# Kernel optimization log

Measured on AMD Instinct MI355X. Metric: run time of the kernel, lower is better.

The kernel has to match this reference:

```python
import jax, jax.numpy as jnp
import numpy as np

N_NODES = 100000
N_EDGES = 3200000
IN_CH = 128
HID = 128
N_CLASSES = 32
N_GRAPHS = 256


def gcn_conv(x, W, b, src, dst, n_nodes):
    """PyG GCNConv: add self-loops, symmetric deg^-1/2 normalization,
    linear transform, gather-scatter aggregation, bias."""
    xw = x @ W  # [N, out]
    loop = jnp.arange(n_nodes, dtype=src.dtype)
    s = jnp.concatenate([src, loop])  # sources incl. self-loops
    d = jnp.concatenate([dst, loop])  # targets incl. self-loops
    deg = jax.ops.segment_sum(jnp.ones_like(d, dtype=xw.dtype), d,
                              num_segments=n_nodes)
    dinv = jnp.where(deg > 0, jax.lax.rsqrt(deg), 0.0)
    norm = dinv[s] * dinv[d]  # [E+N]
    msgs = xw[s] * norm[:, None]  # gather + scale
    out = jax.ops.segment_sum(msgs, d, num_segments=n_nodes)  # scatter-add
    return out + b


def global_mean_pool(x, batch, n_graphs):
    sums = jax.ops.segment_sum(x, batch, num_segments=n_graphs)
    cnt = jax.ops.segment_sum(jnp.ones((x.shape[0],), x.dtype), batch,
                              num_segments=n_graphs)
    return sums / jnp.maximum(cnt, 1.0)[:, None]


def setup_inputs() -> dict:
    key = jax.random.key(0)
    ks = jax.random.split(key, 9)
    x = jax.random.normal(ks[0], (N_NODES, IN_CH), dtype=jnp.float32)
    edge_index = jax.random.randint(ks[1], (2, N_EDGES), 0, N_NODES, dtype=jnp.int32)
    batch = jnp.sort(jax.random.randint(ks[2], (N_NODES,), 0, N_GRAPHS, dtype=jnp.int32))
    s1 = 1.0 / np.sqrt(IN_CH)
    s2 = 1.0 / np.sqrt(HID)
    W1 = jax.random.uniform(ks[3], (IN_CH, HID), jnp.float32, -s1, s1)
    b1 = jnp.zeros((HID,), jnp.float32)
    W2 = jax.random.uniform(ks[4], (HID, HID), jnp.float32, -s2, s2)
    b2 = jnp.zeros((HID,), jnp.float32)
    Wfc = jax.random.uniform(ks[5], (HID, N_CLASSES), jnp.float32, -s2, s2)
    bfc = jax.random.uniform(ks[6], (N_CLASSES,), jnp.float32, -s2, s2)
    return {"x": x, "edge_index": edge_index, "batch": batch,
            "W1": W1, "b1": b1, "W2": W2, "b2": b2, "Wfc": Wfc, "bfc": bfc}


def reference(x, edge_index, batch, W1, b1, W2, b2, Wfc, bfc):
    src, dst = edge_index[0], edge_index[1]
    h = jax.nn.relu(gcn_conv(x, W1, b1, src, dst, N_NODES))
    h = jax.nn.relu(gcn_conv(h, W2, b2, src, dst, N_NODES))
    g = global_mean_pool(h, batch, N_GRAPHS)  # [G, HID]
    return g @ Wfc + bfc  # [G, N_CLASSES]
```

## Files before the change

### kernel.cpp

```cpp
#include <hip/hip_runtime.h>
#include <hip/hip_bf16.h>
#include <hip/hip_fp16.h>

static constexpr int CH     = 128;
static constexpr int NCLS   = 32;
static constexpr int NGRAPH = 256;

static constexpr int BSHIFT = 8;
static constexpr int BW     = 1 << BSHIFT;
static constexpr int MAXB   = 512;

typedef _Float16 half8 __attribute__((ext_vector_type(8)));
typedef _Float16 half4 __attribute__((ext_vector_type(4)));
typedef float    f32x4 __attribute__((ext_vector_type(4)));
typedef float    f32x2 __attribute__((ext_vector_type(2)));

static constexpr float FP8_SCALE = 64.0f;
static constexpr float FP8_INV   = 1.0f / 64.0f;

__device__ __forceinline__ f32x2 dec8(unsigned short u) {
  return __builtin_amdgcn_cvt_pk_f32_fp8((int)u, false);
}
__device__ __forceinline__ unsigned char enc8(float v) {
  return (unsigned char)(__builtin_amdgcn_cvt_pk_fp8_f32(v, v, 0, false) & 0xFF);
}

__global__ __launch_bounds__(256) void k_init_wt(
    int* __restrict__ gcur, int CAP, int NBUCK, int* __restrict__ xzero,
    const float* __restrict__ W1, const float* __restrict__ W2,
    _Float16* __restrict__ WhT1, _Float16* __restrict__ WhT2) {
  int t = threadIdx.x;
  if (blockIdx.x == 0) {
    for (int i = t; i < NBUCK; i += 256) gcur[i] = i * CAP;
    if (t < 32) xzero[t] = 0;
    return;
  }
  int i = (blockIdx.x - 1) * 256 + t;
  const float* W = (i < CH * CH) ? W1 : W2;
  _Float16* T   = (i < CH * CH) ? WhT1 : WhT2;
  int j = i & (CH * CH - 1);
  int k = j >> 7, n = j & 127;
  T[n * CH + k] = (_Float16)W[j];
}

__global__ __launch_bounds__(1024) void k_scatter(
    const int* __restrict__ src, const int* __restrict__ dst,
    int* __restrict__ gcur, int* __restrict__ ebuf, int E) {
  __shared__ int bcnt[MAXB];
  __shared__ int bbase[MAXB];
  int t = threadIdx.x;
  if (t < MAXB) bcnt[t] = 0;
  __syncthreads();
  int base = blockIdx.x * 8192;
  int s_[8], d_[8], r_[8];
  #pragma unroll
  for (int j = 0; j < 8; ++j) {
    int i = base + j * 1024 + t;
    if (i < E) {
      s_[j] = src[i];
      d_[j] = dst[i];
      r_[j] = atomicAdd(&bcnt[d_[j] >> BSHIFT], 1);
    }
  }
  __syncthreads();
  if (t < MAXB && bcnt[t]) bbase[t] = atomicAdd(&gcur[t], bcnt[t]);
  __syncthreads();
  #pragma unroll
  for (int j = 0; j < 8; ++j) {
    int i = base + j * 1024 + t;
    if (i < E) {
      int b = d_[j] >> BSHIFT;
      int p = ((d_[j] & (BW - 1)) << 17) | s_[j];
      ebuf[bbase[b] + r_[j]] = p;
    }
  }
}

__global__ __launch_bounds__(1024) void k_build(
    const int* __restrict__ ebuf, const int* __restrict__ gcur,
    int* __restrict__ offs, int* __restrict__ oend,
    float* __restrict__ dinv, int* __restrict__ csr, int N, int CAP) {
  __shared__ int sdeg[BW];
  __shared__ int sscan[BW];
  int b = blockIdx.x;
  int t = threadIdx.x;
  int lo = b << BSHIFT;
  int e0 = b * CAP;
  int e1 = gcur[b];

  if (t < BW) sdeg[t] = 0;
  __syncthreads();
  for (int e = e0 + t; e < e1; e += 1024)
    atomicAdd(&sdeg[ebuf[e] >> 17], 1);
  __syncthreads();
  if (t < BW) sscan[t] = (sdeg[t] + 3) & ~3;
  __syncthreads();
  for (int st = 1; st < BW; st <<= 1) {
    int v = (t < BW && t >= st) ? sscan[t - st] : 0;
    __syncthreads();
    if (t < BW) sscan[t] += v;
    __syncthreads();
  }
  if (t < BW) {
    int deg  = sdeg[t];
    int pdeg = (deg + 3) & ~3;
    int ex = b * CAP + sscan[t] - pdeg;
    int n = lo + t;
    if (n < N) {
      offs[n] = ex;
      oend[n] = ex + deg;
      dinv[n] = 1.0f / sqrtf((float)(deg + 1));
      for (int q = deg; q < pdeg; ++q) csr[ex + q] = N;
    }
    sscan[t] = ex;
  }
  __syncthreads();
  for (int e = e0 + t; e < e1; e += 1024) {
    int p = ebuf[e];
    int pos = atomicAdd(&sscan[p >> 17], 1);
    csr[pos] = p & 0x1FFFF;
  }
}

__device__ __forceinline__ void stage_w(const _Float16* __restrict__ WhT,
                                        _Float16 (*Ws)[136], int tid) {
  #pragma unroll
  for (int l = 0; l < 8; ++l) {
    int idx = tid + l * 256;
    int n = idx >> 4, k8 = (idx & 15) << 3;
    *(half8*)&Ws[n][k8] = *(const half8*)(WhT + n * CH + k8);
  }
}

__device__ __forceinline__ void gemm_core64(
    const _Float16 (*As)[136], const _Float16 (*Ws)[136],
    const float* __restrict__ dinv, unsigned char* __restrict__ C,
    int row0, int M, int tid) {
  int lane = tid & 63, wave = tid >> 6;
  int quad = lane >> 4, sub = lane & 15;
  int m0 = wave * 16;

  f32x4 acc[8];
  #pragma unroll
  for (int j = 0; j < 8; ++j) acc[j] = (f32x4){0.f, 0.f, 0.f, 0.f};

  #pragma unroll
  for (int kc = 0; kc < 4; ++kc) {
    int ko = kc * 32 + quad * 8;
    half8 a = *(const half8*)&As[m0 + sub][ko];
    #pragma unroll
    for (int nt = 0; nt < 8; ++nt) {
      half8 b = *(const half8*)&Ws[nt * 16 + sub][ko];
      acc[nt] = __builtin_amdgcn_mfma_f32_16x16x32_f16(a, b, acc[nt], 0, 0, 0);
    }
  }
  #pragma unroll
  for (int r = 0; r < 4; ++r) {
    int row = row0 + m0 + quad * 4 + r;
    if (row < M) {
      float d = dinv[row] * FP8_SCALE;
      #pragma unroll
      for (int nt = 0; nt < 8; ++nt)
        C[(size_t)row * CH + nt * 16 + sub] = enc8(acc[nt][r] * d);
    }
  }
}

__global__ __launch_bounds__(256) void k_gemm_f32(
    const float* __restrict__ A, const _Float16* __restrict__ WhT,
    const float* __restrict__ dinv, unsigned char* __restrict__ C, int M) {
  __shared__ _Float16 As[64][136];
  __shared__ _Float16 Ws[128][136];
  int tid = threadIdx.x;
  int row0 = blockIdx.x * 64;
  #pragma unroll
  for (int l = 0; l < 8; ++l) {
    int idx = tid + l * 256;
    int r = idx >> 5, c4 = (idx & 31) << 2;
    int rr = row0 + r; if (rr >= M) rr = M - 1;
    float4 v = *(const float4*)(A + (size_t)rr * CH + c4);
    half4 hv = { (_Float16)v.x, (_Float16)v.y, (_Float16)v.z, (_Float16)v.w };
    *(half4*)&As[r][c4] = hv;
  }
  stage_w(WhT, Ws, tid);
  __syncthreads();
  gemm_core64(As, Ws, dinv, C, row0, M, tid);
}

__global__ __launch_bounds__(256) void k_gemm_f16(
    const _Float16* __restrict__ A, const _Float16* __restrict__ WhT,
    const float* __restrict__ dinv, unsigned char* __restrict__ C, int M) {
  __shared__ _Float16 As[64][136];
  __shared__ _Float16 Ws[128][136];
  int tid = threadIdx.x;
  int row0 = blockIdx.x * 64;
  #pragma unroll
  for (int l = 0; l < 4; ++l) {
    int idx = tid + l * 256;
    int r = idx >> 4, c8 = (idx & 15) << 3;
    int rr = row0 + r; if (rr >= M) rr = M - 1;
    *(half8*)&As[r][c8] = *(const half8*)(A + (size_t)rr * CH + c8);
  }
  stage_w(WhT, Ws, tid);
  __syncthreads();
  gemm_core64(As, Ws, dinv, C, row0, M, tid);
}

__global__ __launch_bounds__(256) void k_agg(
    const unsigned char* __restrict__ xs, const int* __restrict__ csr,
    const int* __restrict__ offs, const int* __restrict__ oend,
    const float* __restrict__ dinv, const float* __restrict__ bias,
    __half* __restrict__ out, int N) {
  int wid0  = blockIdx.x * 4 + (threadIdx.x >> 6);
  int lane  = threadIdx.x & 63;
  int wstep = gridDim.x * 4;
  unsigned int lane2 = (unsigned int)lane << 1;
  float2 bxy = *(const float2*)(bias + 2 * lane);

  auto g = [&](int s) -> unsigned short {
    return *(const unsigned short*)(xs + (((unsigned int)s << 7) | lane2));
  };

  for (int wid = wid0; wid * 2 < N; wid += wstep) {
    int nA = wid * 2, nB = nA + 1;
    bool hasB = (nB < N);

    int eA = offs[nA];
    int cA = (oend[nA] - eA + 3) >> 2;
    int eB = hasB ? offs[nB] : eA;
    int cB = hasB ? ((oend[nB] - eB + 3) >> 2) : 0;

    f32x2 aA0 = dec8(g(nA));
    f32x2 aA1 = {0.f, 0.f};
    f32x2 aB0 = {0.f, 0.f}, aB1 = {0.f, 0.f};
    if (hasB) aB0 = dec8(g(nB));

    if (cA >= 2 && cB >= 2) {
      int4 ca0 = *(const int4*)(csr + eA);
      int4 ca1 = *(const int4*)(csr + eA + 4);
      int4 cb0 = *(const int4*)(csr + eB);
      int4 cb1 = *(const int4*)(csr + eB + 4);
      do {
        unsigned short uA0 = g(ca0.x), uA1 = g(ca0.y), uA2 = g(ca0.z), uA3 = g(ca0.w);
        unsigned short uA4 = g(ca1.x), uA5 = g(ca1.y), uA6 = g(ca1.z), uA7 = g(ca1.w);
        unsigned short uB0 = g(cb0.x), uB1 = g(cb0.y), uB2 = g(cb0.z), uB3 = g(cb0.w);
        unsigned short uB4 = g(cb1.x), uB5 = g(cb1.y), uB6 = g(cb1.z), uB7 = g(cb1.w);
        eA += 8; eB += 8; cA -= 2; cB -= 2;
        int4 na0 = *(const int4*)(csr + eA);
        int4 na1 = *(const int4*)(csr + eA + 4);
        int4 nb0 = *(const int4*)(csr + eB);
        int4 nb1 = *(const int4*)(csr + eB + 4);
        aA0 += dec8(uA0); aA1 += dec8(uA1); aA0 += dec8(uA2); aA1 += dec8(uA3);
        aA0 += dec8(uA4); aA1 += dec8(uA5); aA0 += dec8(uA6); aA1 += dec8(uA7);
        aB0 += dec8(uB0); aB1 += dec8(uB1); aB0 += dec8(uB2); aB1 += dec8(uB3);
        aB0 += dec8(uB4); aB1 += dec8(uB5); aB0 += dec8(uB6); aB1 += dec8(uB7);
        ca0 = na0; ca1 = na1; cb0 = nb0; cb1 = nb1;
      } while (cA >= 2 && cB >= 2);
    }

    auto drain = [&](int e, int c, f32x2& a0, f32x2& a1) {
      while (c >= 2) {
        int4 q0 = *(const int4*)(csr + e);
        int4 q1 = *(const int4*)(csr + e + 4);
        unsigned short u0 = g(q0.x), u1 = g(q0.y), u2 = g(q0.z), u3 = g(q0.w);
        unsigned short u4 = g(q1.x), u5 = g(q1.y), u6 = g(q1.z), u7 = g(q1.w);
        a0 += dec8(u0); a1 += dec8(u1); a0 += dec8(u2); a1 += dec8(u3);
        a0 += dec8(u4); a1 += dec8(u5); a0 += dec8(u6); a1 += dec8(u7);
        e += 8; c -= 2;
      }
      if (c > 0) {
        int4 q0 = *(const int4*)(csr + e);
        unsigned short u0 = g(q0.x), u1 = g(q0.y), u2 = g(q0.z), u3 = g(q0.w);
        a0 += dec8(u0); a1 += dec8(u1); a0 += dec8(u2); a1 += dec8(u3);
      }
    };
    drain(eA, cA, aA0, aA1);
    if (hasB) drain(eB, cB, aB0, aB1);

    {
      f32x2 s = aA0 + aA1;
      float dn = dinv[nA] * FP8_INV;
      float rx = fmaf(s[0], dn, bxy.x);
      float ry = fmaf(s[1], dn, bxy.y);
      ((__half2*)out)[(size_t)nA * 64 + lane] =
          __floats2half2_rn(fmaxf(rx, 0.f), fmaxf(ry, 0.f));
    }
    if (hasB) {
      f32x2 s = aB0 + aB1;
      float dn = dinv[nB] * FP8_INV;
      float rx = fmaf(s[0], dn, bxy.x);
      float ry = fmaf(s[1], dn, bxy.y);
      ((__half2*)out)[(size_t)nB * 64 + lane] =
          __floats2half2_rn(fmaxf(rx, 0.f), fmaxf(ry, 0.f));
    }
  }
}

__global__ __launch_bounds__(128) void k_pool(
    const __half* __restrict__ h, const int* __restrict__ batch,
    float* __restrict__ gsum, int* __restrict__ gstart,
    int* __restrict__ gend, int N) {
  int ch = threadIdx.x;
  int n0 = blockIdx.x * 128;
  int n1 = n0 + 128; if (n1 > N) n1 = N;
  if (n0 >= N) return;
  for (int n = n0 + ch; n < n1; n += 128) {
    int g = batch[n];
    if (n == 0 || batch[n - 1] != g) gstart[g] = n;
    if (n == N - 1 || batch[n + 1] != g) gend[g] = n + 1;
  }
  float acc = 0.f;
  int curg = batch[n0];
  for (int n = n0; n < n1; ++n) {
    int g = batch[n];
    if (g != curg) {
      atomicAdd(&gsum[curg * CH + ch], acc);
      acc = 0.f; curg = g;
    }
    acc += __half2float(h[(size_t)n * CH + ch]);
  }
  atomicAdd(&gsum[curg * CH + ch], acc);
}

__global__ __launch_bounds__(64) void k_fc(
    const float* __restrict__ gsum, const int* __restrict__ gstart,
    const int* __restrict__ gend, const float* __restrict__ Wfc,
    const float* __restrict__ bfc, float* __restrict__ outp) {
  int g = blockIdx.x;
  int j = threadIdx.x;
  if (j >= NCLS) return;
  int cnt = gend[g] - gstart[g];
  float invc = 1.0f / fmaxf((float)cnt, 1.0f);
  float acc = 0.0f;
  for (int c = 0; c < CH; ++c)
    acc = fmaf(gsum[g * CH + c], Wfc[c * NCLS + j], acc);
  outp[g * NCLS + j] = fmaf(acc, invc, bfc[j]);
}

extern "C" void kernel_launch(void* const* d_in, const int* in_sizes, int n_in,
                              void* d_out, int out_size, void* d_ws, size_t ws_size,
                              hipStream_t stream) {
  const float* x    = (const float*)d_in[0];
  const int*   ei   = (const int*)d_in[1];
  const int*   batch= (const int*)d_in[2];
  const float* W1   = (const float*)d_in[3];
  const float* b1   = (const float*)d_in[4];
  const float* W2   = (const float*)d_in[5];
  const float* b2   = (const float*)d_in[6];
  const float* Wfc  = (const float*)d_in[7];
  const float* bfc  = (const float*)d_in[8];
  float* outp = (float*)d_out;

  const int N = in_sizes[0] / CH;
  const int E = in_sizes[1] / 2;
  const int* src = ei;
  const int* dst = ei + E;
  const int NBUCK = (N + BW - 1) >> BSHIFT;
  int CAP = (E / NBUCK) + (E / NBUCK) / 8 + 1280;
  CAP = (CAP + 3) & ~3;

  char* w = (char*)d_ws;
  size_t o = 0;
  auto carve = [&](size_t bytes) -> void* {
    o = (o + 255) & ~(size_t)255;
    void* p = w + o;
    o += bytes;
    return p;
  };
  float*    gsum   = (float*)   carve((size_t)NGRAPH * CH * 4);
  int*      gstart = (int*)     carve((size_t)NGRAPH * 4);
  int*      gend   = (int*)     carve((size_t)NGRAPH * 4);
  size_t zbytes = o;
  int*      offs   = (int*)     carve((size_t)N * 4);
  int*      oendb  = (int*)     carve((size_t)N * 4);
  int*      gcur   = (int*)     carve(MAXB * 4);
  int*      csr    = (int*)     carve((size_t)NBUCK * CAP * 4);
  float*    dinv   = (float*)   carve((size_t)N * 4);
  _Float16* WhT1   = (_Float16*)carve((size_t)CH * CH * 2);
  _Float16* WhT2   = (_Float16*)carve((size_t)CH * CH * 2);
  unsigned char* xsbuf = (unsigned char*)carve((size_t)(N + 1) * CH);
  __half*   hbuf   = (__half*)  carve((size_t)N * CH * 2);
  (void)ws_size;

  int* ebuf = (int*)hbuf;

  (void)hipMemsetAsync(gsum, 0, zbytes, stream);

  const int GB64 = (N + 63) / 64;
  const int GB   = (N + 127) / 128;
  int AB = (N + 7) / 8;
  if (AB > 2048) AB = 2048;

  k_init_wt<<<129, 256, 0, stream>>>(gcur, CAP, NBUCK,
                                     (int*)(xsbuf + (size_t)N * CH),
                                     W1, W2, WhT1, WhT2);
  k_scatter<<<(E + 8191) / 8192, 1024, 0, stream>>>(src, dst, gcur, ebuf, E);
  k_build  <<<NBUCK, 1024, 0, stream>>>(ebuf, gcur, offs, oendb, dinv, csr, N, CAP);

  k_gemm_f32<<<GB64, 256, 0, stream>>>(x, WhT1, dinv, xsbuf, N);
  k_agg<<<AB, 256, 0, stream>>>(xsbuf, csr, offs, oendb, dinv, b1, hbuf, N);
  k_gemm_f16<<<GB64, 256, 0, stream>>>((const _Float16*)hbuf, WhT2, dinv, xsbuf, N);
  k_agg<<<AB, 256, 0, stream>>>(xsbuf, csr, offs, oendb, dinv, b2, hbuf, N);

  k_pool<<<GB, 128, 0, stream>>>(hbuf, batch, gsum, gstart, gend, N);
  k_fc<<<NGRAPH, 64, 0, stream>>>(gsum, gstart, gend, Wfc, bfc, outp);
  (void)out_size; (void)n_in;
}
```

Before: 350.0 us.

## Fuse setup kernels, split edges across half-waves in agg, fuse pool and fc

Removes k_init_wt by folding the weight transpose into k_build and the zeroing into k_scatter. A memset of gcur replaces precomputed bucket bases, and offsets are now relative. The aggregation kernel now has each half-wave process alternate edges with 4-byte gathers (4 fp8 channels per lane), combining the halves with a cross-half shuffle. Pooling and the final FC are fused into one per-graph kernel that uses a binary search on the sorted batch array instead of atomics. This cuts launches and atomics, but the agg path adds shuffles and predicated lanes, and the pool now has only 256 blocks.

```diff
diff --git a/kernel.cpp b/kernel.cpp
--- a/kernel.cpp
+++ b/kernel.cpp
@@ -18,37 +18,18 @@
 static constexpr float FP8_SCALE = 64.0f;
 static constexpr float FP8_INV   = 1.0f / 64.0f;
 
-__device__ __forceinline__ f32x2 dec8(unsigned short u) {
-  return __builtin_amdgcn_cvt_pk_f32_fp8((int)u, false);
-}
 __device__ __forceinline__ unsigned char enc8(float v) {
   return (unsigned char)(__builtin_amdgcn_cvt_pk_fp8_f32(v, v, 0, false) & 0xFF);
 }
 
-__global__ __launch_bounds__(256) void k_init_wt(
-    int* __restrict__ gcur, int CAP, int NBUCK, int* __restrict__ xzero,
-    const float* __restrict__ W1, const float* __restrict__ W2,
-    _Float16* __restrict__ WhT1, _Float16* __restrict__ WhT2) {
-  int t = threadIdx.x;
-  if (blockIdx.x == 0) {
-    for (int i = t; i < NBUCK; i += 256) gcur[i] = i * CAP;
-    if (t < 32) xzero[t] = 0;
-    return;
-  }
-  int i = (blockIdx.x - 1) * 256 + t;
-  const float* W = (i < CH * CH) ? W1 : W2;
-  _Float16* T   = (i < CH * CH) ? WhT1 : WhT2;
-  int j = i & (CH * CH - 1);
-  int k = j >> 7, n = j & 127;
-  T[n * CH + k] = (_Float16)W[j];
-}
-
 __global__ __launch_bounds__(1024) void k_scatter(
     const int* __restrict__ src, const int* __restrict__ dst,
-    int* __restrict__ gcur, int* __restrict__ ebuf, int E) {
+    int* __restrict__ gcur, int* __restrict__ ebuf, int E, int CAP,
+    int* __restrict__ xzero) {
   __shared__ int bcnt[MAXB];
   __shared__ int bbase[MAXB];
   int t = threadIdx.x;
+  if (blockIdx.x == 0 && t < 32) xzero[t] = 0;
   if (t < MAXB) bcnt[t] = 0;
   __syncthreads();
   int base = blockIdx.x * 8192;
@@ -71,7 +52,7 @@
     if (i < E) {
       int b = d_[j] >> BSHIFT;
       int p = ((d_[j] & (BW - 1)) << 17) | s_[j];
-      ebuf[bbase[b] + r_[j]] = p;
+      ebuf[b * CAP + bbase[b] + r_[j]] = p;
     }
   }
 }
@@ -79,14 +60,26 @@
 __global__ __launch_bounds__(1024) void k_build(
     const int* __restrict__ ebuf, const int* __restrict__ gcur,
     int* __restrict__ offs, int* __restrict__ oend,
-    float* __restrict__ dinv, int* __restrict__ csr, int N, int CAP) {
+    float* __restrict__ dinv, int* __restrict__ csr, int N, int CAP,
+    const float* __restrict__ W1, const float* __restrict__ W2,
+    _Float16* __restrict__ WhT1, _Float16* __restrict__ WhT2) {
   __shared__ int sdeg[BW];
   __shared__ int sscan[BW];
   int b = blockIdx.x;
   int t = threadIdx.x;
+
+  int gi = b * 1024 + t;
+  if (gi < 2 * CH * CH) {
+    const float* W = (gi < CH * CH) ? W1 : W2;
+    _Float16* T   = (gi < CH * CH) ? WhT1 : WhT2;
+    int j = gi & (CH * CH - 1);
+    int k = j >> 7, n = j & 127;
+    T[n * CH + k] = (_Float16)W[j];
+  }
+
   int lo = b << BSHIFT;
   int e0 = b * CAP;
-  int e1 = gcur[b];
+  int e1 = e0 + gcur[b];
 
   if (t < BW) sdeg[t] = 0;
   __syncthreads();
@@ -207,18 +200,19 @@
 }
 
 __global__ __launch_bounds__(256) void k_agg(
-    const unsigned char* __restrict__ xs, const int* __restrict__ csr,
+    const unsigned int* __restrict__ xs32, const int* __restrict__ csr,
     const int* __restrict__ offs, const int* __restrict__ oend,
     const float* __restrict__ dinv, const float* __restrict__ bias,
     __half* __restrict__ out, int N) {
+  int lane  = threadIdx.x & 63;
   int wid0  = blockIdx.x * 4 + (threadIdx.x >> 6);
-  int lane  = threadIdx.x & 63;
   int wstep = gridDim.x * 4;
-  unsigned int lane2 = (unsigned int)lane << 1;
-  float2 bxy = *(const float2*)(bias + 2 * lane);
-
-  auto g = [&](int s) -> unsigned short {
-    return *(const unsigned short*)(xs + (((unsigned int)s << 7) | lane2));
+  int e = lane >> 5;
+  unsigned int c = lane & 31;
+  float4 bb = *(const float4*)(bias + c * 4);
+
+  auto G = [&](int s) -> unsigned int {
+    return xs32[((unsigned int)s << 5) | c];
   };
 
   for (int wid = wid0; wid * 2 < N; wid += wstep) {
@@ -230,10 +224,22 @@
     int eB = hasB ? offs[nB] : eA;
     int cB = hasB ? ((oend[nB] - eB + 3) >> 2) : 0;
 
-    f32x2 aA0 = dec8(g(nA));
-    f32x2 aA1 = {0.f, 0.f};
-    f32x2 aB0 = {0.f, 0.f}, aB1 = {0.f, 0.f};
-    if (hasB) aB0 = dec8(g(nB));
+    f32x2 a0 = {0.f, 0.f}, a1 = {0.f, 0.f};
+    f32x2 b0 = {0.f, 0.f}, b1 = {0.f, 0.f};
+    if (e == 0) {
+      unsigned int ow = G(nA);
+      a0 = __builtin_amdgcn_cvt_pk_f32_fp8((int)ow, false);
+      a1 = __builtin_amdgcn_cvt_pk_f32_fp8((int)ow, true);
+      if (hasB) {
+        unsigned int ob = G(nB);
+        b0 = __builtin_amdgcn_cvt_pk_f32_fp8((int)ob, false);
+        b1 = __builtin_amdgcn_cvt_pk_f32_fp8((int)ob, true);
+      }
+    }
+
+    #define ACC(d, x0, x1) \
+      x0 += __builtin_amdgcn_cvt_pk_f32_fp8((int)(d), false); \
+      x1 += __builtin_amdgcn_cvt_pk_f32_fp8((int)(d), true);
 
     if (cA >= 2 && cB >= 2) {
       int4 ca0 = *(const int4*)(csr + eA);
@@ -241,100 +247,115 @@
       int4 cb0 = *(const int4*)(csr + eB);
       int4 cb1 = *(const int4*)(csr + eB + 4);
       do {
-        unsigned short uA0 = g(ca0.x), uA1 = g(ca0.y), uA2 = g(ca0.z), uA3 = g(ca0.w);
-        unsigned short uA4 = g(ca1.x), uA5 = g(ca1.y), uA6 = g(ca1.z), uA7 = g(ca1.w);
-        unsigned short uB0 = g(cb0.x), uB1 = g(cb0.y), uB2 = g(cb0.z), uB3 = g(cb0.w);
-        unsigned short uB4 = g(cb1.x), uB5 = g(cb1.y), uB6 = g(cb1.z), uB7 = g(cb1.w);
+        int sA0 = e ? ca0.y : ca0.x, sA1 = e ? ca0.w : ca0.z;
+        int sA2 = e ? ca1.y : ca1.x, sA3 = e ? ca1.w : ca1.z;
+        int sB0 = e ? cb0.y : cb0.x, sB1 = e ? cb0.w : cb0.z;
+        int sB2 = e ? cb1.y : cb1.x, sB3 = e ? cb1.w : cb1.z;
+        unsigned int dA0 = G(sA0), dA1 = G(sA1), dA2 = G(sA2), dA3 = G(sA3);
+        unsigned int dB0 = G(sB0), dB1 = G(sB1), dB2 = G(sB2), dB3 = G(sB3);
         eA += 8; eB += 8; cA -= 2; cB -= 2;
         int4 na0 = *(const int4*)(csr + eA);
         int4 na1 = *(const int4*)(csr + eA + 4);
         int4 nb0 = *(const int4*)(csr + eB);
         int4 nb1 = *(const int4*)(csr + eB + 4);
-        aA0 += dec8(uA0); aA1 += dec8(uA1); aA0 += dec8(uA2); aA1 += dec8(uA3);
-        aA0 += dec8(uA4); aA1 += dec8(uA5); aA0 += dec8(uA6); aA1 += dec8(uA7);
-        aB0 += dec8(uB0); aB1 += dec8(uB1); aB0 += dec8(uB2); aB1 += dec8(uB3);
-        aB0 += dec8(uB4); aB1 += dec8(uB5); aB0 += dec8(uB6); aB1 += dec8(uB7);
+        ACC(dA0, a0, a1); ACC(dA1, a0, a1); ACC(dA2, a0, a1); ACC(dA3, a0, a1);
+        ACC(dB0, b0, b1); ACC(dB1, b0, b1); ACC(dB2, b0, b1); ACC(dB3, b0, b1);
         ca0 = na0; ca1 = na1; cb0 = nb0; cb1 = nb1;
       } while (cA >= 2 && cB >= 2);
     }
 
-    auto drain = [&](int e, int c, f32x2& a0, f32x2& a1) {
-      while (c >= 2) {
-        int4 q0 = *(const int4*)(csr + e);
-        int4 q1 = *(const int4*)(csr + e + 4);
-        unsigned short u0 = g(q0.x), u1 = g(q0.y), u2 = g(q0.z), u3 = g(q0.w);
-        unsigned short u4 = g(q1.x), u5 = g(q1.y), u6 = g(q1.z), u7 = g(q1.w);
-        a0 += dec8(u0); a1 += dec8(u1); a0 += dec8(u2); a1 += dec8(u3);
-        a0 += dec8(u4); a1 += dec8(u5); a0 += dec8(u6); a1 += dec8(u7);
-        e += 8; c -= 2;
+    auto drain = [&](int ee, int cc, f32x2& x0, f32x2& x1) {
+      while (cc >= 2) {
+        int4 q0 = *(const int4*)(csr + ee);
+        int4 q1 = *(const int4*)(csr + ee + 4);
+        int s0 = e ? q0.y : q0.x, s1 = e ? q0.w : q0.z;
+        int s2 = e ? q1.y : q1.x, s3 = e ? q1.w : q1.z;
+        unsigned int d0 = G(s0), d1 = G(s1), d2 = G(s2), d3 = G(s3);
+        ACC(d0, x0, x1); ACC(d1, x0, x1); ACC(d2, x0, x1); ACC(d3, x0, x1);
+        ee += 8; cc -= 2;
       }
-      if (c > 0) {
-        int4 q0 = *(const int4*)(csr + e);
-        unsigned short u0 = g(q0.x), u1 = g(q0.y), u2 = g(q0.z), u3 = g(q0.w);
-        a0 += dec8(u0); a1 += dec8(u1); a0 += dec8(u2); a1 += dec8(u3);
+      if (cc > 0) {
+        int4 q0 = *(const int4*)(csr + ee);
+        int s0 = e ? q0.y : q0.x, s1 = e ? q0.w : q0.z;
+        unsigned int d0 = G(s0), d1 = G(s1);
+        ACC(d0, x0, x1); ACC(d1, x0, x1);
       }
     };
-    drain(eA, cA, aA0, aA1);
-    if (hasB) drain(eB, cB, aB0, aB1);
-
-    {
-      f32x2 s = aA0 + aA1;
-      float dn = dinv[nA] * FP8_INV;
-      float rx = fmaf(s[0], dn, bxy.x);
-      float ry = fmaf(s[1], dn, bxy.y);
-      ((__half2*)out)[(size_t)nA * 64 + lane] =
-          __floats2half2_rn(fmaxf(rx, 0.f), fmaxf(ry, 0.f));
-    }
+    drain(eA, cA, a0, a1);
+    if (hasB) drain(eB, cB, b0, b1);
+    #undef ACC
+
+    a0[0] += __shfl_xor(a0[0], 32); a0[1] += __shfl_xor(a0[1], 32);
+    a1[0] += __shfl_xor(a1[0], 32); a1[1] += __shfl_xor(a1[1], 32);
     if (hasB) {
-      f32x2 s = aB0 + aB1;
-      float dn = dinv[nB] * FP8_INV;
-      float rx = fmaf(s[0], dn, bxy.x);
-      float ry = fmaf(s[1], dn, bxy.y);
-      ((__half2*)out)[(size_t)nB * 64 + lane] =
-          __floats2half2_rn(fmaxf(rx, 0.f), fmaxf(ry, 0.f));
-    }
-  }
-}
-
-__global__ __launch_bounds__(128) void k_pool(
+      b0[0] += __shfl_xor(b0[0], 32); b0[1] += __shfl_xor(b0[1], 32);
+      b1[0] += __shfl_xor(b1[0], 32); b1[1] += __shfl_xor(b1[1], 32);
+    }
+
+    if (e == 0) {
+      {
+        float dn = dinv[nA] * FP8_INV;
+        float r0 = fmaf(a0[0], dn, bb.x), r1 = fmaf(a0[1], dn, bb.y);
+        float r2 = fmaf(a1[0], dn, bb.z), r3 = fmaf(a1[1], dn, bb.w);
+        __half2 h0 = __floats2half2_rn(fmaxf(r0, 0.f), fmaxf(r1, 0.f));
+        __half2 h1 = __floats2half2_rn(fmaxf(r2, 0.f), fmaxf(r3, 0.f));
+        __half2* op = (__half2*)(out + (size_t)nA * CH + c * 4);
+        op[0] = h0; op[1] = h1;
+      }
+      if (hasB) {
+        float dn = dinv[nB] * FP8_INV;
+        float r0 = fmaf(b0[0], dn, bb.x), r1 = fmaf(b0[1], dn, bb.y);
+        float r2 = fmaf(b1[0], dn, bb.z), r3 = fmaf(b1[1], dn, bb.w);
+        __half2 h0 = __floats2half2_rn(fmaxf(r0, 0.f), fmaxf(r1, 0.f));
+        __half2 h1 = __floats2half2_rn(fmaxf(r2, 0.f), fmaxf(r3, 0.f));
+        __half2* op = (__half2*)(out + (size_t)nB * CH + c * 4);
+        op[0] = h0; op[1] = h1;
+      }
+    }
+  }
+}
+
+__global__ __launch_bounds__(256) void k_poolfc(
     const __half* __restrict__ h, const int* __restrict__ batch,
-    float* __restrict__ gsum, int* __restrict__ gstart,
-    int* __restrict__ gend, int N) {
-  int ch = threadIdx.x;
-  int n0 = blockIdx.x * 128;
-  int n1 = n0 + 128; if (n1 > N) n1 = N;
-  if (n0 >= N) return;
-  for (int n = n0 + ch; n < n1; n += 128) {
-    int g = batch[n];
-    if (n == 0 || batch[n - 1] != g) gstart[g] = n;
-    if (n == N - 1 || batch[n + 1] != g) gend[g] = n + 1;
-  }
-  float acc = 0.f;
-  int curg = batch[n0];
-  for (int n = n0; n < n1; ++n) {
-    int g = batch[n];
-    if (g != curg) {
-      atomicAdd(&gsum[curg * CH + ch], acc);
-      acc = 0.f; curg = g;
-    }
-    acc += __half2float(h[(size_t)n * CH + ch]);
-  }
-  atomicAdd(&gsum[curg * CH + ch], acc);
-}
-
-__global__ __launch_bounds__(64) void k_fc(
-    const float* __restrict__ gsum, const int* __restrict__ gstart,
-    const int* __restrict__ gend, const float* __restrict__ Wfc,
-    const float* __restrict__ bfc, float* __restrict__ outp) {
+    const float* __restrict__ Wfc, const float* __restrict__ bfc,
+    float* __restrict__ outp, int N) {
+  __shared__ float sred[256][2];
+  __shared__ float gs[CH];
   int g = blockIdx.x;
-  int j = threadIdx.x;
-  if (j >= NCLS) return;
-  int cnt = gend[g] - gstart[g];
-  float invc = 1.0f / fmaxf((float)cnt, 1.0f);
-  float acc = 0.0f;
-  for (int c = 0; c < CH; ++c)
-    acc = fmaf(gsum[g * CH + c], Wfc[c * NCLS + j], acc);
-  outp[g * NCLS + j] = fmaf(acc, invc, bfc[j]);
+  int t = threadIdx.x;
+
+  int lo = 0, hi = N;
+  while (lo < hi) { int m = (lo + hi) >> 1; if (batch[m] < g) lo = m + 1; else hi = m; }
+  int s0 = lo;
+  hi = N;
+  while (lo < hi) { int m = (lo + hi) >> 1; if (batch[m] < g + 1) lo = m + 1; else hi = m; }
+  int s1 = lo;
+
+  int ch2 = t & 63;
+  int rh  = t >> 6;
+  const __half2* h2 = (const __half2*)h;
+  float ax = 0.f, ay = 0.f;
+  for (int n = s0 + rh; n < s1; n += 4) {
+    float2 v = __half22float2(h2[(size_t)n * 64 + ch2]);
+    ax += v.x; ay += v.y;
+  }
+  sred[t][0] = ax; sred[t][1] = ay;
+  __syncthreads();
+  if (t < 64) {
+    float invc = 1.0f / fmaxf((float)(s1 - s0), 1.0f);
+    float sx = sred[t][0] + sred[t + 64][0] + sred[t + 128][0] + sred[t + 192][0];
+    float sy = sred[t][1] + sred[t + 64][1] + sred[t + 128][1] + sred[t + 192][1];
+    gs[2 * t]     = sx * invc;
+    gs[2 * t + 1] = sy * invc;
+  }
+  __syncthreads();
+  if (t < NCLS) {
+    float acc = bfc[t];
+    #pragma unroll 8
+    for (int cc = 0; cc < CH; ++cc)
+      acc = fmaf(gs[cc], Wfc[cc * NCLS + t], acc);
+    outp[g * NCLS + t] = acc;
+  }
 }
 
 extern "C" void kernel_launch(void* const* d_in, const int* in_sizes, int n_in,
@@ -367,10 +388,6 @@
     o += bytes;
     return p;
   };
-  float*    gsum   = (float*)   carve((size_t)NGRAPH * CH * 4);
-  int*      gstart = (int*)     carve((size_t)NGRAPH * 4);
-  int*      gend   = (int*)     carve((size_t)NGRAPH * 4);
-  size_t zbytes = o;
   int*      offs   = (int*)     carve((size_t)N * 4);
   int*      oendb  = (int*)     carve((size_t)N * 4);
   int*      gcur   = (int*)     carve(MAXB * 4);
@@ -384,25 +401,24 @@
 
   int* ebuf = (int*)hbuf;
 
-  (void)hipMemsetAsync(gsum, 0, zbytes, stream);
+  (void)hipMemsetAsync(gcur, 0, MAXB * 4, stream);
 
   const int GB64 = (N + 63) / 64;
-  const int GB   = (N + 127) / 128;
   int AB = (N + 7) / 8;
   if (AB > 2048) AB = 2048;
 
-  k_init_wt<<<129, 256, 0, stream>>>(gcur, CAP, NBUCK,
-                                     (int*)(xsbuf + (size_t)N * CH),
-                                     W1, W2, WhT1, WhT2);
-  k_scatter<<<(E + 8191) / 8192, 1024, 0, stream>>>(src, dst, gcur, ebuf, E);
-  k_build  <<<NBUCK, 1024, 0, stream>>>(ebuf, gcur, offs, oendb, dinv, csr, N, CAP);
+  k_scatter<<<(E + 8191) / 8192, 1024, 0, stream>>>(
+      src, dst, gcur, ebuf, E, CAP, (int*)(xsbuf + (size_t)N * CH));
+  k_build<<<NBUCK, 1024, 0, stream>>>(ebuf, gcur, offs, oendb, dinv, csr,
+                                      N, CAP, W1, W2, WhT1, WhT2);
 
   k_gemm_f32<<<GB64, 256, 0, stream>>>(x, WhT1, dinv, xsbuf, N);
-  k_agg<<<AB, 256, 0, stream>>>(xsbuf, csr, offs, oendb, dinv, b1, hbuf, N);
+  k_agg<<<AB, 256, 0, stream>>>((const unsigned int*)xsbuf, csr, offs, oendb,
+                                dinv, b1, hbuf, N);
   k_gemm_f16<<<GB64, 256, 0, stream>>>((const _Float16*)hbuf, WhT2, dinv, xsbuf, N);
-  k_agg<<<AB, 256, 0, stream>>>(xsbuf, csr, offs, oendb, dinv, b2, hbuf, N);
-
-  k_pool<<<GB, 128, 0, stream>>>(hbuf, batch, gsum, gstart, gend, N);
-  k_fc<<<NGRAPH, 64, 0, stream>>>(gsum, gstart, gend, Wfc, bfc, outp);
+  k_agg<<<AB, 256, 0, stream>>>((const unsigned int*)xsbuf, csr, offs, oendb,
+                                dinv, b2, hbuf, N);
+
+  k_poolfc<<<NGRAPH, 256, 0, stream>>>(hbuf, batch, Wfc, bfc, outp, N);
   (void)out_size; (void)n_in;
 }
```

After: 333.4 us. 4.8% less time.
